# Kernel tuning notes

Hardware: AMD Instinct MI355X
Metric: run time of the kernel (lower is better)

Reference implementation:

```python
import jax, jax.numpy as jnp
import numpy as np

N, D, P, R, T, K = 200000, 128, 4096, 4, 3, 16

def setup_inputs() -> dict:
    key = jax.random.key(0)
    ks = jax.random.split(key, 9)
    return {
        "node_embeds": jax.random.normal(ks[0], (N, D), jnp.float32),
        "node_pairs": jax.random.randint(ks[1], (P, 2), 0, N),
        "node_type_ids": jax.random.randint(ks[2], (N,), 0, T),
        "neighbor_idx": jax.random.randint(ks[3], (P, 2, R, K), 0, N),
        "delta_t": jax.random.uniform(ks[4], (P, 2, R, K), jnp.float32),
        "W_phi": jax.random.normal(ks[5], (T, D, D), jnp.float32) * 0.05,
        "W_zeta": jax.random.normal(ks[6], (2 * D,), jnp.float32) * 0.05,
        "W_beta_w": jax.random.normal(ks[7], (R, D, D), jnp.float32) * 0.05,
        "W_beta_b": jax.random.normal(ks[8], (R, D), jnp.float32) * 0.05,
    }

def reference(node_embeds, node_pairs, node_type_ids, neighbor_idx, delta_t,
              W_phi, W_zeta, W_beta_w, W_beta_b):
    n = node_embeds.shape[0]
    # per-node type-specific linear: compute all types then select (T small)
    H_all = jnp.einsum('nd,tde->tne', node_embeds, W_phi)        # [T,N,D]
    H = H_all[node_type_ids, jnp.arange(n)]                      # [N,D]
    # micro attention: e = W_zeta([h_n; h_s]) * exp(-dt), softmax over K neighbors
    zn, zs = W_zeta[:D], W_zeta[D:]
    h_n = H[neighbor_idx]                                        # [P,2,R,K,D]
    e_n = jnp.einsum('psrkd,d->psrk', h_n, zn)
    e_s = jnp.einsum('psd,d->ps', H[node_pairs], zs)             # [P,2]
    e = (e_n + e_s[:, :, None, None]) * jnp.exp(-delta_t)        # [P,2,R,K]
    alpha = jax.nn.softmax(e, axis=-1)
    # meso: attention-weighted aggregation per relation, then per-relation linear
    h_nei = node_embeds[neighbor_idx]                            # [P,2,R,K,D]
    h_agg = jnp.einsum('psrk,psrkd->psrd', alpha, h_nei)         # [P,2,R,D]
    h_beta = jnp.einsum('psrd,rde->psre', h_agg, W_beta_w) + W_beta_b
    # macro: average over both pair sides and relations, sigmoid combine
    x_tilde = h_beta.mean(axis=(1, 2))                           # [P,D]
    return jax.nn.sigmoid(x_tilde)
```

## Files before the change

### kernel.cpp

```cpp
#include <hip/hip_runtime.h>
#include <hip/hip_bf16.h>

#define NN 200000
#define D 128
#define P 4096
#define R 4
#define T 3
#define K 16

__device__ __forceinline__ float bf2f(unsigned int u) {
    union { unsigned int i; float f; } c;
    c.i = u << 16;
    return c.f;
}
__device__ __forceinline__ unsigned short f2bf(float x) {
    union { float f; unsigned int i; } c; c.f = x;
    unsigned int r = c.i + 0x7FFFu + ((c.i >> 16) & 1u);
    return (unsigned short)(r >> 16);
}
__device__ __forceinline__ float ldE(const void* p, size_t i, int f32) {
    return f32 ? ((const float*)p)[i] : bf2f(((const unsigned short*)p)[i]);
}
__device__ __forceinline__ void ld8(const void* p, size_t off, int f32, float* o) {
    if (f32) {
        const float* q = (const float*)p + off;
        float4 a = *(const float4*)q;
        float4 b = *(const float4*)(q + 4);
        o[0]=a.x; o[1]=a.y; o[2]=a.z; o[3]=a.w;
        o[4]=b.x; o[5]=b.y; o[6]=b.z; o[7]=b.w;
    } else {
        uint4 r = *(const uint4*)((const unsigned short*)p + off);
        o[0]=bf2f(r.x & 0xffffu); o[1]=bf2f(r.x >> 16);
        o[2]=bf2f(r.y & 0xffffu); o[3]=bf2f(r.y >> 16);
        o[4]=bf2f(r.z & 0xffffu); o[5]=bf2f(r.z >> 16);
        o[6]=bf2f(r.w & 0xffffu); o[7]=bf2f(r.w >> 16);
    }
}
__device__ __forceinline__ float readlane_f(float v, int lane) {
    return __int_as_float(__builtin_amdgcn_readlane(__float_as_int(v), lane));
}

__global__ void prep_kernel(const unsigned short* __restrict__ emb_u,
                            const void* __restrict__ W_phi,
                            const void* __restrict__ W_zeta,
                            int* __restrict__ gflag,
                            float* __restrict__ ws_v, float* __restrict__ ws_u) {
    __shared__ int sbad[2];
    const int tid = threadIdx.x;
    const int t   = blockIdx.x;
    int bad = 0;
    #pragma unroll
    for (int i = 0; i < 4; ++i) {
        unsigned short u = emb_u[(size_t)(blockIdx.x * 512 + tid * 4 + i) * 2 * 97];
        unsigned int e = (u >> 7) & 0xFFu;
        if (e >= 147u) bad = 1;
    }
    int anyb = __any(bad) ? 1 : 0;
    if ((tid & 63) == 0) sbad[tid >> 6] = anyb;
    __syncthreads();
    const int f32 = sbad[0] | sbad[1];
    if (t == 0 && tid == 0) *gflag = f32;

    const int d = tid;
    const size_t rb = (size_t)(t * D + d) * D;
    float av = 0.f, au = 0.f;
    for (int e = 0; e < D; e += 8) {
        float w[8], zn[8], zs[8];
        ld8(W_phi, rb + e, f32, w);
        ld8(W_zeta, e, f32, zn);
        ld8(W_zeta, D + e, f32, zs);
        #pragma unroll
        for (int q = 0; q < 8; ++q) { av += w[q] * zn[q]; au += w[q] * zs[q]; }
    }
    ws_v[t * D + d] = av;
    ws_u[t * D + d] = au;
}

__global__ __launch_bounds__(256) void precompute_c(
    const void* __restrict__ emb, const int* __restrict__ types,
    const float* __restrict__ ws_v, const float* __restrict__ ws_u,
    const int* __restrict__ flag,
    float* __restrict__ c, float* __restrict__ c2)
{
    __shared__ float vsh[T * D], ush[T * D];
    const int f32 = *flag;
    const int tid = threadIdx.x;
    for (int i = tid; i < T * D; i += 256) { vsh[i] = ws_v[i]; ush[i] = ws_u[i]; }
    __syncthreads();
    const int w = tid >> 6, l = tid & 63;
    const int grp = l >> 4, ch = l & 15;
    const int nbase = blockIdx.x * 64 + w * 4 + grp;

    int   tt[4];
    float rv[4][8];
    #pragma unroll
    for (int it = 0; it < 4; ++it) {
        int n = nbase + it * 16;
        tt[it] = types[n];
        ld8(emb, (size_t)n * D + ch * 8, f32, rv[it]);
    }
    #pragma unroll
    for (int it = 0; it < 4; ++it) {
        int n = nbase + it * 16;
        const float* vp = vsh + tt[it] * D + ch * 8;
        const float* up = ush + tt[it] * D + ch * 8;
        float a = 0.f, b = 0.f;
        #pragma unroll
        for (int q = 0; q < 8; ++q) { a += rv[it][q] * vp[q]; b += rv[it][q] * up[q]; }
        #pragma unroll
        for (int off = 1; off <= 8; off <<= 1) {
            a += __shfl_xor(a, off, 64);
            b += __shfl_xor(b, off, 64);
        }
        if (ch == 0) { c[n] = a; c2[n] = b; }
    }
}

__global__ __launch_bounds__(256, 4) void fused_all(
    const void* __restrict__ emb,
    const int* __restrict__ pairs,
    const int* __restrict__ nbr,
    const void* __restrict__ dlt,
    const void* __restrict__ W_bw,
    const void* __restrict__ W_bb,
    const float* __restrict__ c,
    const float* __restrict__ c2,
    const int* __restrict__ flag,
    void* __restrict__ out)
{
    __shared__ __align__(16) float gsh[2][2][R][D];
    __shared__ __align__(16) float ysh[2][2][D];

    const int f32  = *flag;
    const int tid  = threadIdx.x;
    const int wv   = tid >> 6;
    const int l    = tid & 63;
    const int pr   = wv >> 1;
    const int s    = wv & 1;
    const int p    = blockIdx.x * 2 + pr;
    const int rsub = l >> 4;
    const int ch   = l & 15;
    const int base = p * 2 * R * K + s * 64;

    const int   nb = nbr[base + l];
    const float dt = ldE(dlt, (size_t)base + l, f32);
    const float ce = c[nb];
    const float es = c2[pairs[p * 2 + s]];
    float e = (ce + es) * __expf(-dt);
    float m = e;
    #pragma unroll
    for (int off = 1; off <= 8; off <<= 1) m = fmaxf(m, __shfl_xor(m, off, 64));
    float al = __expf(e - m);
    float ssum = al;
    #pragma unroll
    for (int off = 1; off <= 8; off <<= 1) ssum += __shfl_xor(ssum, off, 64);
    al *= (1.f / ssum);

    if (!f32) {
        const unsigned short* eu = (const unsigned short*)emb;
        #pragma unroll
        for (int r = 0; r < R; ++r) {
            unsigned int ud[K];
            #pragma unroll
            for (int k = 0; k < K; ++k) {
                int s_nb = __builtin_amdgcn_readlane(nb, r * K + k);
                ud[k] = *(const unsigned int*)(eu + (size_t)s_nb * D + 2 * l);
            }
            float a0 = 0.f, a1 = 0.f;
            #pragma unroll
            for (int k = 0; k < K; ++k) {
                float a = readlane_f(al, r * K + k);
                a0 += a * bf2f(ud[k] & 0xffffu);
                a1 += a * bf2f(ud[k] >> 16);
            }
            gsh[pr][s][r][2 * l]     = a0;
            gsh[pr][s][r][2 * l + 1] = a1;
        }
    } else {
        const float* ef = (const float*)emb;
        #pragma unroll
        for (int r = 0; r < R; ++r) {
            float2 ud[K];
            #pragma unroll
            for (int k = 0; k < K; ++k) {
                int s_nb = __builtin_amdgcn_readlane(nb, r * K + k);
                ud[k] = *(const float2*)(ef + (size_t)s_nb * D + 2 * l);
            }
            float a0 = 0.f, a1 = 0.f;
            #pragma unroll
            for (int k = 0; k < K; ++k) {
                float a = readlane_f(al, r * K + k);
                a0 += a * ud[k].x;
                a1 += a * ud[k].y;
            }
            gsh[pr][s][r][2 * l]     = a0;
            gsh[pr][s][r][2 * l + 1] = a1;
        }
    }
    __syncthreads();

    float y[8] = {0.f,0.f,0.f,0.f,0.f,0.f,0.f,0.f};
    const unsigned short* Wu = (const unsigned short*)W_bw;
    #pragma unroll
    for (int rr = 0; rr < 2; ++rr) {
        const int r = s * 2 + rr;
        #pragma unroll 8
        for (int dd = 0; dd < 32; ++dd) {
            const int d = rsub * 32 + dd;
            float gd = gsh[pr][0][r][d] + gsh[pr][1][r][d];
            size_t wo = ((size_t)(r * D + d)) * D + ch * 8;
            if (!f32) {
                uint4 wr = *(const uint4*)(Wu + wo);
                y[0] += gd * bf2f(wr.x & 0xffffu); y[1] += gd * bf2f(wr.x >> 16);
                y[2] += gd * bf2f(wr.y & 0xffffu); y[3] += gd * bf2f(wr.y >> 16);
                y[4] += gd * bf2f(wr.z & 0xffffu); y[5] += gd * bf2f(wr.z >> 16);
                y[6] += gd * bf2f(wr.w & 0xffffu); y[7] += gd * bf2f(wr.w >> 16);
            } else {
                float wb[8]; ld8(W_bw, wo, 1, wb);
                #pragma unroll
                for (int q = 0; q < 8; ++q) y[q] += gd * wb[q];
            }
        }
    }
    #pragma unroll
    for (int q = 0; q < 8; ++q) {
        y[q] += __shfl_xor(y[q], 16, 64);
        y[q] += __shfl_xor(y[q], 32, 64);
    }
    if (rsub == 0) {
        *(float4*)(&ysh[pr][s][ch * 8])     = make_float4(y[0], y[1], y[2], y[3]);
        *(float4*)(&ysh[pr][s][ch * 8 + 4]) = make_float4(y[4], y[5], y[6], y[7]);
    }
    __syncthreads();

    if (s == 0 && rsub == 0) {
        float bs[8] = {0.f,0.f,0.f,0.f,0.f,0.f,0.f,0.f};
        #pragma unroll
        for (int r = 0; r < R; ++r) {
            float bb[8]; ld8(W_bb, (size_t)r * D + ch * 8, f32, bb);
            #pragma unroll
            for (int q = 0; q < 8; ++q) bs[q] += bb[q];
        }
        float o[8];
        #pragma unroll
        for (int q = 0; q < 8; ++q) {
            int e2 = ch * 8 + q;
            float x = (ysh[pr][0][e2] + ysh[pr][1][e2] + 2.f * bs[q]) * 0.125f;
            o[q] = 1.f / (1.f + __expf(-x));
        }
        size_t ob = (size_t)p * D + ch * 8;
        if (f32) {
            *(float4*)((float*)out + ob)     = make_float4(o[0], o[1], o[2], o[3]);
            *(float4*)((float*)out + ob + 4) = make_float4(o[4], o[5], o[6], o[7]);
        } else {
            uint4 pk;
            pk.x = (unsigned int)f2bf(o[0]) | ((unsigned int)f2bf(o[1]) << 16);
            pk.y = (unsigned int)f2bf(o[2]) | ((unsigned int)f2bf(o[3]) << 16);
            pk.z = (unsigned int)f2bf(o[4]) | ((unsigned int)f2bf(o[5]) << 16);
            pk.w = (unsigned int)f2bf(o[6]) | ((unsigned int)f2bf(o[7]) << 16);
            *(uint4*)((unsigned short*)out + ob) = pk;
        }
    }
}

extern "C" void kernel_launch(void* const* d_in, const int* in_sizes, int n_in,
                              void* d_out, int out_size, void* d_ws, size_t ws_size,
                              hipStream_t stream) {
    const void* emb    = d_in[0];
    const int*  pairs  = (const int*)d_in[1];
    const int*  types  = (const int*)d_in[2];
    const int*  nbr    = (const int*)d_in[3];
    const void* dlt    = d_in[4];
    const void* W_phi  = d_in[5];
    const void* W_zeta = d_in[6];
    const void* W_bw   = d_in[7];
    const void* W_bb   = d_in[8];

    int*   flag = (int*)d_ws;
    float* ws_v = (float*)d_ws + 64;
    float* ws_u = ws_v + T * D;
    float* c    = (float*)d_ws + 1024;
    float* c2   = c + NN;

    prep_kernel<<<dim3(T), dim3(128), 0, stream>>>((const unsigned short*)emb,
                                                   W_phi, W_zeta, flag, ws_v, ws_u);
    precompute_c<<<dim3(NN / 64), dim3(256), 0, stream>>>(emb, types, ws_v, ws_u,
                                                          flag, c, c2);
    fused_all<<<dim3(P / 2), dim3(256), 0, stream>>>(emb, pairs, nbr, dlt,
                                                     W_bw, W_bb, c, c2, flag, d_out);
}
```

Baseline: 261.5 us.

## Gather neighbor rows with 16-byte loads and double-buffer across relations

The neighbor gather is restructured. Each lane now loads 8 contiguous bf16 values (uint4) from 4 neighbors instead of 4-byte loads from all 16 neighbors. Partial sums are reduced across the lane groups with xor shuffles, and the loads for the next relation are prefetched while the current one is accumulated. Launch bounds drop from 4 to 2 blocks per SM to allow the extra registers the prefetch buffers need. The trade-off is that extra shuffles and lower occupancy replace the many narrow scattered loads.

```diff
diff --git a/kernel.cpp b/kernel.cpp
--- a/kernel.cpp
+++ b/kernel.cpp
@@ -35,9 +35,6 @@
         o[4]=bf2f(r.z & 0xffffu); o[5]=bf2f(r.z >> 16);
         o[6]=bf2f(r.w & 0xffffu); o[7]=bf2f(r.w >> 16);
     }
-}
-__device__ __forceinline__ float readlane_f(float v, int lane) {
-    return __int_as_float(__builtin_amdgcn_readlane(__float_as_int(v), lane));
 }
 
 __global__ void prep_kernel(const unsigned short* __restrict__ emb_u,
@@ -116,7 +113,7 @@
     }
 }
 
-__global__ __launch_bounds__(256, 4) void fused_all(
+__global__ __launch_bounds__(256, 2) void fused_all(
     const void* __restrict__ emb,
     const int* __restrict__ pairs,
     const int* __restrict__ nbr,
@@ -158,43 +155,78 @@
 
     if (!f32) {
         const unsigned short* eu = (const unsigned short*)emb;
+        int snb[4];
+        uint4 cur[4], nxt[4];
+        #pragma unroll
+        for (int i = 0; i < 4; ++i) snb[i] = __shfl(nb, i * 4 + rsub, 64);
+        #pragma unroll
+        for (int i = 0; i < 4; ++i)
+            cur[i] = *(const uint4*)(eu + (size_t)snb[i] * D + ch * 8);
+
         #pragma unroll
         for (int r = 0; r < R; ++r) {
-            unsigned int ud[K];
-            #pragma unroll
-            for (int k = 0; k < K; ++k) {
-                int s_nb = __builtin_amdgcn_readlane(nb, r * K + k);
-                ud[k] = *(const unsigned int*)(eu + (size_t)s_nb * D + 2 * l);
-            }
-            float a0 = 0.f, a1 = 0.f;
-            #pragma unroll
-            for (int k = 0; k < K; ++k) {
-                float a = readlane_f(al, r * K + k);
-                a0 += a * bf2f(ud[k] & 0xffffu);
-                a1 += a * bf2f(ud[k] >> 16);
-            }
-            gsh[pr][s][r][2 * l]     = a0;
-            gsh[pr][s][r][2 * l + 1] = a1;
+            if (r < 3) {
+                #pragma unroll
+                for (int i = 0; i < 4; ++i)
+                    snb[i] = __shfl(nb, (r + 1) * 16 + i * 4 + rsub, 64);
+                #pragma unroll
+                for (int i = 0; i < 4; ++i)
+                    nxt[i] = *(const uint4*)(eu + (size_t)snb[i] * D + ch * 8);
+            }
+            float av[4];
+            #pragma unroll
+            for (int i = 0; i < 4; ++i) av[i] = __shfl(al, r * 16 + i * 4 + rsub, 64);
+
+            float acc[8] = {0.f,0.f,0.f,0.f,0.f,0.f,0.f,0.f};
+            #pragma unroll
+            for (int i = 0; i < 4; ++i) {
+                float a = av[i];
+                acc[0] += a * bf2f(cur[i].x & 0xffffu); acc[1] += a * bf2f(cur[i].x >> 16);
+                acc[2] += a * bf2f(cur[i].y & 0xffffu); acc[3] += a * bf2f(cur[i].y >> 16);
+                acc[4] += a * bf2f(cur[i].z & 0xffffu); acc[5] += a * bf2f(cur[i].z >> 16);
+                acc[6] += a * bf2f(cur[i].w & 0xffffu); acc[7] += a * bf2f(cur[i].w >> 16);
+            }
+            #pragma unroll
+            for (int q = 0; q < 8; ++q) {
+                acc[q] += __shfl_xor(acc[q], 16, 64);
+                acc[q] += __shfl_xor(acc[q], 32, 64);
+            }
+            if (rsub == 0) {
+                *(float4*)(&gsh[pr][s][r][ch * 8])     = make_float4(acc[0], acc[1], acc[2], acc[3]);
+                *(float4*)(&gsh[pr][s][r][ch * 8 + 4]) = make_float4(acc[4], acc[5], acc[6], acc[7]);
+            }
+            #pragma unroll
+            for (int i = 0; i < 4; ++i) cur[i] = nxt[i];
         }
     } else {
-        const float* ef = (const float*)emb;
+        const float* efp = (const float*)emb;
         #pragma unroll
         for (int r = 0; r < R; ++r) {
-            float2 ud[K];
-            #pragma unroll
-            for (int k = 0; k < K; ++k) {
-                int s_nb = __builtin_amdgcn_readlane(nb, r * K + k);
-                ud[k] = *(const float2*)(ef + (size_t)s_nb * D + 2 * l);
-            }
-            float a0 = 0.f, a1 = 0.f;
-            #pragma unroll
-            for (int k = 0; k < K; ++k) {
-                float a = readlane_f(al, r * K + k);
-                a0 += a * ud[k].x;
-                a1 += a * ud[k].y;
-            }
-            gsh[pr][s][r][2 * l]     = a0;
-            gsh[pr][s][r][2 * l + 1] = a1;
+            int snb[4]; float av[4];
+            #pragma unroll
+            for (int i = 0; i < 4; ++i) {
+                int srcl = r * 16 + i * 4 + rsub;
+                snb[i] = __shfl(nb, srcl, 64);
+                av[i]  = __shfl(al, srcl, 64);
+            }
+            float acc[8] = {0.f,0.f,0.f,0.f,0.f,0.f,0.f,0.f};
+            #pragma unroll
+            for (int i = 0; i < 4; ++i) {
+                float4 r0 = *(const float4*)(efp + (size_t)snb[i] * D + ch * 8);
+                float4 r1 = *(const float4*)(efp + (size_t)snb[i] * D + ch * 8 + 4);
+                float a = av[i];
+                acc[0] += a * r0.x; acc[1] += a * r0.y; acc[2] += a * r0.z; acc[3] += a * r0.w;
+                acc[4] += a * r1.x; acc[5] += a * r1.y; acc[6] += a * r1.z; acc[7] += a * r1.w;
+            }
+            #pragma unroll
+            for (int q = 0; q < 8; ++q) {
+                acc[q] += __shfl_xor(acc[q], 16, 64);
+                acc[q] += __shfl_xor(acc[q], 32, 64);
+            }
+            if (rsub == 0) {
+                *(float4*)(&gsh[pr][s][r][ch * 8])     = make_float4(acc[0], acc[1], acc[2], acc[3]);
+                *(float4*)(&gsh[pr][s][r][ch * 8 + 4]) = make_float4(acc[4], acc[5], acc[6], acc[7]);
+            }
         }
     }
     __syncthreads();
```

Result: no change. 264.1 us (+1.0%).

## Stage neighbor rows into LDS via async global-to-LDS loads, one pair per block

Applied to the files above, without the earlier changes.

The fused kernel now processes one pair per 128-thread block instead of two pairs per 256-thread block. In bf16 mode it issues async 16-byte global_load_lds gathers of all 64 neighbor rows into shared memory before the softmax math, so the loads overlap with the attention computation. In fp32 mode it switches to float4 row gathers with cross-lane reduction. The aggregated features are stored as bf16 in shared memory to halve LDS use, which adds rounding error relative to the fp32 accumulation it replaces. Launch bounds also change, which affects occupancy.

```diff
diff --git a/kernel.cpp b/kernel.cpp
--- a/kernel.cpp
+++ b/kernel.cpp
@@ -38,6 +38,17 @@
 }
 __device__ __forceinline__ float readlane_f(float v, int lane) {
     return __int_as_float(__builtin_amdgcn_readlane(__float_as_int(v), lane));
+}
+
+__device__ __forceinline__ void async_gather16(const void* gptr, void* ldsptr) {
+#if defined(__HIP_DEVICE_COMPILE__) && __has_builtin(__builtin_amdgcn_global_load_lds)
+    __builtin_amdgcn_global_load_lds(
+        (const __attribute__((address_space(1))) void*)gptr,
+        (__attribute__((address_space(3))) void*)ldsptr, 16, 0, 0);
+#else
+    const uint4 v = *(const uint4*)gptr;
+    ((uint4*)ldsptr)[threadIdx.x & 63] = v;
+#endif
 }
 
 __global__ void prep_kernel(const unsigned short* __restrict__ emb_u,
@@ -116,7 +127,7 @@
     }
 }
 
-__global__ __launch_bounds__(256, 4) void fused_all(
+__global__ __launch_bounds__(128, 2) void fused_all(
     const void* __restrict__ emb,
     const int* __restrict__ pairs,
     const int* __restrict__ nbr,
@@ -128,21 +139,30 @@
     const int* __restrict__ flag,
     void* __restrict__ out)
 {
-    __shared__ __align__(16) float gsh[2][2][R][D];
-    __shared__ __align__(16) float ysh[2][2][D];
+    __shared__ __align__(16) unsigned short srow[2][R * K][D];
+    __shared__ __align__(16) unsigned short gshb[2][R][D];
+    __shared__ __align__(16) float ysh[2][D];
 
     const int f32  = *flag;
     const int tid  = threadIdx.x;
-    const int wv   = tid >> 6;
+    const int s    = tid >> 6;
     const int l    = tid & 63;
-    const int pr   = wv >> 1;
-    const int s    = wv & 1;
-    const int p    = blockIdx.x * 2 + pr;
+    const int p    = blockIdx.x;
     const int rsub = l >> 4;
     const int ch   = l & 15;
     const int base = p * 2 * R * K + s * 64;
 
-    const int   nb = nbr[base + l];
+    const int nb = nbr[base + l];
+
+    if (!f32) {
+        const unsigned short* eu = (const unsigned short*)emb;
+        #pragma unroll
+        for (int t = 0; t < 16; ++t) {
+            int nbq = __shfl(nb, t * 4 + (l >> 4), 64);
+            async_gather16(eu + (size_t)nbq * D + ch * 8, &srow[s][t * 4][0]);
+        }
+    }
+
     const float dt = ldE(dlt, (size_t)base + l, f32);
     const float ce = c[nb];
     const float es = c2[pairs[p * 2 + s]];
@@ -157,44 +177,51 @@
     al *= (1.f / ssum);
 
     if (!f32) {
-        const unsigned short* eu = (const unsigned short*)emb;
+        __syncthreads();
         #pragma unroll
         for (int r = 0; r < R; ++r) {
-            unsigned int ud[K];
-            #pragma unroll
-            for (int k = 0; k < K; ++k) {
-                int s_nb = __builtin_amdgcn_readlane(nb, r * K + k);
-                ud[k] = *(const unsigned int*)(eu + (size_t)s_nb * D + 2 * l);
-            }
             float a0 = 0.f, a1 = 0.f;
             #pragma unroll
             for (int k = 0; k < K; ++k) {
                 float a = readlane_f(al, r * K + k);
-                a0 += a * bf2f(ud[k] & 0xffffu);
-                a1 += a * bf2f(ud[k] >> 16);
-            }
-            gsh[pr][s][r][2 * l]     = a0;
-            gsh[pr][s][r][2 * l + 1] = a1;
+                unsigned int d2 = *(const unsigned int*)&srow[s][r * K + k][2 * l];
+                a0 += a * bf2f(d2 & 0xffffu);
+                a1 += a * bf2f(d2 >> 16);
+            }
+            *(unsigned int*)&gshb[s][r][2 * l] =
+                (unsigned int)f2bf(a0) | ((unsigned int)f2bf(a1) << 16);
         }
     } else {
-        const float* ef = (const float*)emb;
+        const float* efp = (const float*)emb;
         #pragma unroll
         for (int r = 0; r < R; ++r) {
-            float2 ud[K];
-            #pragma unroll
-            for (int k = 0; k < K; ++k) {
-                int s_nb = __builtin_amdgcn_readlane(nb, r * K + k);
-                ud[k] = *(const float2*)(ef + (size_t)s_nb * D + 2 * l);
-            }
-            float a0 = 0.f, a1 = 0.f;
-            #pragma unroll
-            for (int k = 0; k < K; ++k) {
-                float a = readlane_f(al, r * K + k);
-                a0 += a * ud[k].x;
-                a1 += a * ud[k].y;
-            }
-            gsh[pr][s][r][2 * l]     = a0;
-            gsh[pr][s][r][2 * l + 1] = a1;
+            int snb[4]; float av4[4];
+            #pragma unroll
+            for (int i = 0; i < 4; ++i) {
+                int srcl = r * 16 + i * 4 + rsub;
+                snb[i] = __shfl(nb, srcl, 64);
+                av4[i] = __shfl(al, srcl, 64);
+            }
+            float acc[8] = {0.f,0.f,0.f,0.f,0.f,0.f,0.f,0.f};
+            #pragma unroll
+            for (int i = 0; i < 4; ++i) {
+                float4 r0 = *(const float4*)(efp + (size_t)snb[i] * D + ch * 8);
+                float4 r1 = *(const float4*)(efp + (size_t)snb[i] * D + ch * 8 + 4);
+                float a = av4[i];
+                acc[0] += a * r0.x; acc[1] += a * r0.y; acc[2] += a * r0.z; acc[3] += a * r0.w;
+                acc[4] += a * r1.x; acc[5] += a * r1.y; acc[6] += a * r1.z; acc[7] += a * r1.w;
+            }
+            #pragma unroll
+            for (int q = 0; q < 8; ++q) {
+                acc[q] += __shfl_xor(acc[q], 16, 64);
+                acc[q] += __shfl_xor(acc[q], 32, 64);
+            }
+            if (rsub == 0) {
+                #pragma unroll
+                for (int q = 0; q < 4; ++q)
+                    *(unsigned int*)&gshb[s][r][ch * 8 + 2 * q] =
+                        (unsigned int)f2bf(acc[2 * q]) | ((unsigned int)f2bf(acc[2 * q + 1]) << 16);
+            }
         }
     }
     __syncthreads();
@@ -207,7 +234,7 @@
         #pragma unroll 8
         for (int dd = 0; dd < 32; ++dd) {
             const int d = rsub * 32 + dd;
-            float gd = gsh[pr][0][r][d] + gsh[pr][1][r][d];
+            float gd = bf2f(gshb[0][r][d]) + bf2f(gshb[1][r][d]);
             size_t wo = ((size_t)(r * D + d)) * D + ch * 8;
             if (!f32) {
                 uint4 wr = *(const uint4*)(Wu + wo);
@@ -228,8 +255,8 @@
         y[q] += __shfl_xor(y[q], 32, 64);
     }
     if (rsub == 0) {
-        *(float4*)(&ysh[pr][s][ch * 8])     = make_float4(y[0], y[1], y[2], y[3]);
-        *(float4*)(&ysh[pr][s][ch * 8 + 4]) = make_float4(y[4], y[5], y[6], y[7]);
+        *(float4*)(&ysh[s][ch * 8])     = make_float4(y[0], y[1], y[2], y[3]);
+        *(float4*)(&ysh[s][ch * 8 + 4]) = make_float4(y[4], y[5], y[6], y[7]);
     }
     __syncthreads();
 
@@ -245,7 +272,7 @@
         #pragma unroll
         for (int q = 0; q < 8; ++q) {
             int e2 = ch * 8 + q;
-            float x = (ysh[pr][0][e2] + ysh[pr][1][e2] + 2.f * bs[q]) * 0.125f;
+            float x = (ysh[0][e2] + ysh[1][e2] + 2.f * bs[q]) * 0.125f;
             o[q] = 1.f / (1.f + __expf(-x));
         }
         size_t ob = (size_t)p * D + ch * 8;
@@ -286,6 +313,6 @@
                                                    W_phi, W_zeta, flag, ws_v, ws_u);
     precompute_c<<<dim3(NN / 64), dim3(256), 0, stream>>>(emb, types, ws_v, ws_u,
                                                           flag, c, c2);
-    fused_all<<<dim3(P / 2), dim3(256), 0, stream>>>(emb, pairs, nbr, dlt,
-                                                     W_bw, W_bb, c, c2, flag, d_out);
-}
+    fused_all<<<dim3(P), dim3(128), 0, stream>>>(emb, pairs, nbr, dlt,
+                                                 W_bw, W_bb, c, c2, flag, d_out);
+}
```

After: 328.2 us. +25.5%, slower.
